# Kernel optimization log

Hardware: AMD Instinct MI355X
Metric: run time of the kernel (lower is better)

Reference implementation:

```python
import jax, jax.numpy as jnp
import numpy as np

V, E, H, L, T, B = 50257, 1024, 16, 12, 128, 16
FF = 4 * E
STD = 0.02


def setup_inputs() -> dict:
    key = jax.random.key(0)
    ks = jax.random.split(key, 20)
    n = lambda k, shape: (jax.random.normal(k, shape, dtype=jnp.float32) * STD)
    inp = {
        'idx': jax.random.randint(ks[0], (B, T), 0, V, dtype=jnp.int64),
        'targets': jax.random.randint(ks[1], (B, T), 0, V, dtype=jnp.int64),
        'tok_emb': n(ks[2], (V, E)),
        'pos_emb': n(ks[3], (T, E)),
        'wq': n(ks[4], (L, E, E)),
        'wk': n(ks[5], (L, E, E)),
        'wv': n(ks[6], (L, E, E)),
        'w_proj': n(ks[7], (L, E, E)),
        'b_proj': jnp.zeros((L, E), jnp.float32),
        'ln1_g': jnp.ones((L, E), jnp.float32),
        'ln1_b': jnp.zeros((L, E), jnp.float32),
        'ln2_g': jnp.ones((L, E), jnp.float32),
        'ln2_b': jnp.zeros((L, E), jnp.float32),
        'w_fc1': n(ks[8], (L, E, FF)),
        'b_fc1': jnp.zeros((L, FF), jnp.float32),
        'w_fc2': n(ks[9], (L, FF, E)),
        'b_fc2': jnp.zeros((L, E), jnp.float32),
        'lnf_g': jnp.ones((E,), jnp.float32),
        'lnf_b': jnp.zeros((E,), jnp.float32),
        'w_head': n(ks[10], (E, V)),
        'b_head': jnp.zeros((V,), jnp.float32),
    }
    return inp


def _layernorm(x, g, b, eps=1e-5):
    m = x.mean(-1, keepdims=True)
    v = ((x - m) ** 2).mean(-1, keepdims=True)
    return (x - m) / jnp.sqrt(v + eps) * g + b


def _forward(idx, targets, tok_emb, pos_emb, wq, wk, wv, w_proj, b_proj,
             ln1_g, ln1_b, ln2_g, ln2_b, w_fc1, b_fc1, w_fc2, b_fc2,
             lnf_g, lnf_b, w_head, b_head):
    Bb, Tt = idx.shape
    x = tok_emb[idx] + pos_emb[:Tt]  # (B, T, E)
    causal = jnp.tril(jnp.ones((Tt, Tt), dtype=bool))
    scale = E ** (-0.5)  # NOTE: original scales by full n_embd, not head_size

    def block(x, p):
        (wq_l, wk_l, wv_l, wp_l, bp_l, g1, b1, g2, b2, wf1, bf1, wf2, bf2) = p
        h = _layernorm(x, g1, b1)
        q = (h @ wq_l).reshape(Bb, Tt, H, -1)
        k = (h @ wk_l).reshape(Bb, Tt, H, -1)
        v = (h @ wv_l).reshape(Bb, Tt, H, -1)
        sc = jnp.einsum('bthd,bshd->bhts', q, k) * scale
        sc = jnp.where(causal, sc, -jnp.inf)
        att = jax.nn.softmax(sc, axis=-1)
        o = jnp.einsum('bhts,bshd->bthd', att, v).reshape(Bb, Tt, E)
        x = x + o @ wp_l + bp_l
        h2 = _layernorm(x, g2, b2)
        x = x + jax.nn.relu(h2 @ wf1 + bf1) @ wf2 + bf2
        return x, None

    x, _ = jax.lax.scan(block, x, (wq, wk, wv, w_proj, b_proj, ln1_g, ln1_b,
                                   ln2_g, ln2_b, w_fc1, b_fc1, w_fc2, b_fc2))
    x = _layernorm(x, lnf_g, lnf_b)
    logits = x @ w_head + b_head  # (B, T, V)
    logp = jax.nn.log_softmax(logits, axis=-1)
    nll = -jnp.take_along_axis(logp.reshape(Bb * Tt, -1),
                               targets.reshape(-1, 1), axis=1)
    loss = nll.mean()
    return logits, loss


def reference(idx, targets, tok_emb, pos_emb, wq, wk, wv, w_proj, b_proj,
              ln1_g, ln1_b, ln2_g, ln2_b, w_fc1, b_fc1, w_fc2, b_fc2,
              lnf_g, lnf_b, w_head, b_head):
    return _forward(idx, targets, tok_emb, pos_emb, wq, wk, wv, w_proj, b_proj,
                    ln1_g, ln1_b, ln2_g, ln2_b, w_fc1, b_fc1, w_fc2, b_fc2,
                    lnf_g, lnf_b, w_head, b_head)
```

## Files before the change

### kernel.cpp

```cpp
#include <hip/hip_runtime.h>
#include <math.h>

typedef unsigned short u16;
typedef float f32x4 __attribute__((ext_vector_type(4)));
typedef short bf16x8 __attribute__((ext_vector_type(8)));
typedef unsigned short us4 __attribute__((ext_vector_type(4)));

#define DEVI __device__ __forceinline__

DEVI float bf2f(u16 u) { return __uint_as_float(((unsigned int)u) << 16); }
DEVI u16 f2bf(float f) {
    unsigned int u = __float_as_uint(f);
    u += 0x7fffu + ((u >> 16) & 1u);
    return (u16)(u >> 16);
}

__global__ __launch_bounds__(256) void k_embed(const int* __restrict__ idx,
                                               const float* __restrict__ te,
                                               const float* __restrict__ pe,
                                               float* __restrict__ x) {
    int m = blockIdx.x;
    int t = m & 127;
    int tok = idx[m];
    const f32x4* a = (const f32x4*)(te + (long)tok * 1024);
    const f32x4* p = (const f32x4*)(pe + (long)t * 1024);
    f32x4* o = (f32x4*)(x + (long)m * 1024);
    o[threadIdx.x] = a[threadIdx.x] + p[threadIdx.x];
}

__global__ __launch_bounds__(256) void k_ln(const float* __restrict__ x,
                                            const float* __restrict__ g,
                                            const float* __restrict__ b,
                                            u16* __restrict__ out) {
    __shared__ float red[8];
    int tid = threadIdx.x, lane = tid & 63, wid = tid >> 6;
    int r = blockIdx.x;
    f32x4 v = ((const f32x4*)(x + (long)r * 1024))[tid];
    float s = v.x + v.y + v.z + v.w;
#pragma unroll
    for (int o2 = 32; o2; o2 >>= 1) s += __shfl_xor(s, o2);
    if (lane == 0) red[wid] = s;
    __syncthreads();
    float mean = (red[0] + red[1] + red[2] + red[3]) * (1.0f / 1024.0f);
    f32x4 d; d.x = v.x - mean; d.y = v.y - mean; d.z = v.z - mean; d.w = v.w - mean;
    float sq = d.x * d.x + d.y * d.y + d.z * d.z + d.w * d.w;
#pragma unroll
    for (int o2 = 32; o2; o2 >>= 1) sq += __shfl_xor(sq, o2);
    if (lane == 0) red[4 + wid] = sq;
    __syncthreads();
    float rstd = rsqrtf((red[4] + red[5] + red[6] + red[7]) * (1.0f / 1024.0f) + 1e-5f);
    f32x4 gg = ((const f32x4*)g)[tid];
    f32x4 bb = ((const f32x4*)b)[tid];
    us4 o4;
    o4.x = f2bf(d.x * rstd * gg.x + bb.x);
    o4.y = f2bf(d.y * rstd * gg.y + bb.y);
    o4.z = f2bf(d.z * rstd * gg.z + bb.z);
    o4.w = f2bf(d.w * rstd * gg.w + bb.w);
    ((us4*)(out + (long)r * 1024))[tid] = o4;
}

DEVI void tr_tile(const float* __restrict__ in, u16* __restrict__ out,
                  int K, int N, int k0, int n0, int tid, float (*tile)[65]) {
    int trow = tid >> 4;
    int tcol = (tid & 15) * 4;
#pragma unroll
    for (int p = 0; p < 4; ++p) {
        int k = k0 + trow + p * 16;
        const float* src = in + (long)k * N + n0 + tcol;
#pragma unroll
        for (int j = 0; j < 4; ++j) {
            int n = n0 + tcol + j;
            tile[trow + p * 16][tcol + j] = (n < N) ? src[j] : 0.0f;
        }
    }
    __syncthreads();
#pragma unroll
    for (int p = 0; p < 4; ++p) {
        int n = n0 + trow + p * 16;
        if (n < N) {
            us4 o4;
#pragma unroll
            for (int j = 0; j < 4; ++j) o4[j] = f2bf(tile[tcol + j][trow + p * 16]);
            *(us4*)(out + (long)n * K + k0 + tcol) = o4;
        }
    }
}

__global__ __launch_bounds__(256) void k_tr_one(const float* __restrict__ in,
                                                u16* __restrict__ out, int K, int N) {
    __shared__ float tile[64][65];
    tr_tile(in, out, K, N, blockIdx.y * 64, blockIdx.x * 64, threadIdx.x, tile);
}

__global__ __launch_bounds__(256) void k_tr_layer(
    const float* __restrict__ wq, const float* __restrict__ wk,
    const float* __restrict__ wv, const float* __restrict__ wp,
    const float* __restrict__ f1, const float* __restrict__ f2,
    u16* __restrict__ oqkv, u16* __restrict__ oproj,
    u16* __restrict__ of1, u16* __restrict__ of2) {
    __shared__ float tile[64][65];
    int id = blockIdx.x;
    const float* in; u16* out; int K, N, txx, tyy;
    if (id < 1024) {
        int t = id >> 8, s2 = id & 255;
        txx = s2 & 15; tyy = s2 >> 4; K = 1024; N = 1024;
        in = (t == 0) ? wq : (t == 1) ? wk : (t == 2) ? wv : wp;
        out = (t == 3) ? oproj : oqkv + (long)t * 1024 * 1024;
    } else if (id < 2048) {
        int s2 = id - 1024;
        txx = s2 & 63; tyy = s2 >> 6; K = 1024; N = 4096; in = f1; out = of1;
    } else {
        int s2 = id - 2048;
        txx = s2 & 15; tyy = s2 >> 4; K = 4096; N = 1024; in = f2; out = of2;
    }
    tr_tile(in, out, K, N, tyy * 64, txx * 64, threadIdx.x, tile);
}

template <int ROWS>
DEVI void stage_tile(const u16* __restrict__ g, long row0, long rowmax, int ld,
                     int col0, char* lds, int tid) {
    constexpr int NCH = ROWS * 8;
#pragma unroll
    for (int p = 0; p < NCH / 256; ++p) {
        int c = tid + p * 256;
        int row = c >> 3;
        int gslot = c & 7;
        int gdata = gslot ^ (row & 7);
        long gr = row0 + row;
        if (gr > rowmax) gr = rowmax;
        const u16* src = g + gr * (long)ld + col0 + gdata * 8;
        char* dst = lds + ((long)((tid & 192) + p * 256)) * 16;
        __builtin_amdgcn_global_load_lds(
            (const __attribute__((address_space(1))) void*)src,
            (__attribute__((address_space(3))) void*)dst, 16, 0, 0);
    }
}

template <int BN, bool OUT_BF16, bool RELU, bool HAS_BIAS, bool HAS_RES>
__global__ __launch_bounds__(256, 3) void k_gemm(
    const u16* __restrict__ A, const u16* __restrict__ Bt,
    const float* __restrict__ bias, const float* __restrict__ res,
    float* __restrict__ Cf, u16* __restrict__ Cb,
    int M, int N, int K, int ldc) {
    constexpr int NR = BN / 32;
    constexpr int ASZ = 128 * 64 * 2;
    constexpr int BSZ = BN * 64 * 2;
    __shared__ __align__(16) char lds[2 * (ASZ + BSZ)];
    int tid = threadIdx.x, lane = tid & 63, wid = tid >> 6;
    int l15 = lane & 15, l4 = lane >> 4;
    int wr = wid >> 1, wc = wid & 1;
    long m0 = (long)blockIdx.y * 128;
    long n0 = (long)blockIdx.x * BN;
    f32x4 acc[4][NR] = {};
    const int nk = K >> 6;

    stage_tile<128>(A, m0, (long)M - 1, K, 0, lds, tid);
    stage_tile<BN>(Bt, n0, (long)N - 1, K, 0, lds + ASZ, tid);
    int cur = 0;
    for (int kt = 0; kt < nk; ++kt) {
        __syncthreads();
        if (kt + 1 < nk) {
            char* nb = lds + (cur ^ 1) * (ASZ + BSZ);
            stage_tile<128>(A, m0, (long)M - 1, K, (kt + 1) << 6, nb, tid);
            stage_tile<BN>(Bt, n0, (long)N - 1, K, (kt + 1) << 6, nb + ASZ, tid);
        }
        const char* ab = lds + cur * (ASZ + BSZ);
        const char* bb = ab + ASZ;
#pragma unroll
        for (int kh = 0; kh < 2; ++kh) {
            bf16x8 af[4], bfv[NR];
#pragma unroll
            for (int mi = 0; mi < 4; ++mi) {
                int row = wr * 64 + mi * 16 + l15;
                int slot = (kh * 4 + l4) ^ (row & 7);
                af[mi] = *(const bf16x8*)(ab + (row * 8 + slot) * 16);
            }
#pragma unroll
            for (int ni = 0; ni < NR; ++ni) {
                int row = wc * (BN / 2) + ni * 16 + l15;
                int slot = (kh * 4 + l4) ^ (row & 7);
                bfv[ni] = *(const bf16x8*)(bb + (row * 8 + slot) * 16);
            }
#pragma unroll
            for (int mi = 0; mi < 4; ++mi)
#pragma unroll
                for (int ni = 0; ni < NR; ++ni)
                    acc[mi][ni] = __builtin_amdgcn_mfma_f32_16x16x32_bf16(
                        af[mi], bfv[ni], acc[mi][ni], 0, 0, 0);
        }
        cur ^= 1;
    }
#pragma unroll
    for (int ni = 0; ni < NR; ++ni) {
        long n = n0 + wc * (BN / 2) + ni * 16 + l15;
        if (n < N) {
            float bv = HAS_BIAS ? bias[n] : 0.0f;
#pragma unroll
            for (int mi = 0; mi < 4; ++mi) {
#pragma unroll
                for (int j = 0; j < 4; ++j) {
                    long m = m0 + wr * 64 + mi * 16 + l4 * 4 + j;
                    float v = acc[mi][ni][j] + bv;
                    if (HAS_RES) v += res[m * (long)ldc + n];
                    if (RELU) v = fmaxf(v, 0.0f);
                    if (OUT_BF16) Cb[m * (long)ldc + n] = f2bf(v);
                    else Cf[m * (long)ldc + n] = v;
                }
            }
        }
    }
}

__global__ __launch_bounds__(256, 2) void k_head128(
    const u16* __restrict__ A, const u16* __restrict__ Bt,
    const float* __restrict__ bias, float* __restrict__ Cf,
    float2* __restrict__ part, int M, int N, int K, int ldc) {
    constexpr int ASZ = 128 * 64 * 2;
    constexpr int BSZ = 128 * 64 * 2;
    __shared__ __align__(16) char lds[128 * 129 * 4];
    int tid = threadIdx.x, lane = tid & 63, wid = tid >> 6;
    int l15 = lane & 15, l4 = lane >> 4;
    int wr = wid >> 1, wc = wid & 1;
    int bn = blockIdx.x, bm = blockIdx.y;
    long m0 = (long)bm * 128, n0 = (long)bn * 128;
    f32x4 acc[4][4] = {};
    const int nk = K >> 6;

    stage_tile<128>(A, m0, (long)M - 1, K, 0, lds, tid);
    stage_tile<128>(Bt, n0, (long)N - 1, K, 0, lds + ASZ, tid);
    int cur = 0;
    for (int kt = 0; kt < nk; ++kt) {
        __syncthreads();
        if (kt + 1 < nk) {
            char* nb = lds + (cur ^ 1) * (ASZ + BSZ);
            stage_tile<128>(A, m0, (long)M - 1, K, (kt + 1) << 6, nb, tid);
            stage_tile<128>(Bt, n0, (long)N - 1, K, (kt + 1) << 6, nb + ASZ, tid);
        }
        const char* ab = lds + cur * (ASZ + BSZ);
        const char* bb = ab + ASZ;
#pragma unroll
        for (int kh = 0; kh < 2; ++kh) {
            bf16x8 af[4], bfv[4];
#pragma unroll
            for (int mi = 0; mi < 4; ++mi) {
                int row = wr * 64 + mi * 16 + l15;
                int slot = (kh * 4 + l4) ^ (row & 7);
                af[mi] = *(const bf16x8*)(ab + (row * 8 + slot) * 16);
            }
#pragma unroll
            for (int ni = 0; ni < 4; ++ni) {
                int row = wc * 64 + ni * 16 + l15;
                int slot = (kh * 4 + l4) ^ (row & 7);
                bfv[ni] = *(const bf16x8*)(bb + (row * 8 + slot) * 16);
            }
#pragma unroll
            for (int mi = 0; mi < 4; ++mi)
#pragma unroll
                for (int ni = 0; ni < 4; ++ni)
                    acc[mi][ni] = __builtin_amdgcn_mfma_f32_16x16x32_bf16(
                        af[mi], bfv[ni], acc[mi][ni], 0, 0, 0);
        }
        cur ^= 1;
    }
    const float BIG_NEG = -1e30f;
    float bvv[4];
#pragma unroll
    for (int ni = 0; ni < 4; ++ni) {
        long n = n0 + wc * 64 + ni * 16 + l15;
        bvv[ni] = (n < N) ? bias[n] : 0.0f;
    }
    __syncthreads();
    float* ldsF = (float*)lds;
#pragma unroll
    for (int mi = 0; mi < 4; ++mi)
#pragma unroll
        for (int ni = 0; ni < 4; ++ni)
#pragma unroll
            for (int j = 0; j < 4; ++j) {
                int row = wr * 64 + mi * 16 + l4 * 4 + j;
                int col = wc * 64 + ni * 16 + l15;
                long n = n0 + col;
                float v = acc[mi][ni][j] + bvv[ni];
                if (n >= N) v = BIG_NEG;
                ldsF[row * 129 + col] = v;
            }
    __syncthreads();
#pragma unroll 4
    for (int i = 0; i < 64; ++i) {
        int flat = tid + (i << 8);
        int row = flat >> 7, col = flat & 127;
        long n = n0 + col;
        if (n < N)
            __builtin_nontemporal_store(ldsF[row * 129 + col],
                                        &Cf[(m0 + row) * (long)ldc + n]);
    }
    {
        int r = tid >> 1, half = tid & 1;
        const float* rp = ldsF + r * 129 + half * 64;
        float mx = BIG_NEG;
#pragma unroll 8
        for (int c = 0; c < 64; ++c) mx = fmaxf(mx, rp[c]);
        float sm = 0.f;
#pragma unroll 8
        for (int c = 0; c < 64; ++c) sm += __expf(rp[c] - mx);
        float mo = __shfl_xor(mx, 1), so = __shfl_xor(sm, 1);
        float nm = fmaxf(mx, mo);
        float S = sm * __expf(mx - nm) + so * __expf(mo - nm);
        if (half == 0)
            part[(long)bn * M + m0 + r] = make_float2(nm, S);
    }
}

__global__ __launch_bounds__(256) void k_attn_mfma(const u16* __restrict__ qkv,
                                                   u16* __restrict__ o) {
    __shared__ __align__(16) u16 Ks[128 * 64];
    __shared__ __align__(16) u16 Vt[64 * 128];
    __shared__ __align__(16) u16 Ps[4][32 * 128];
    int tid = threadIdx.x, lane = tid & 63, w = tid >> 6;
    int l15 = lane & 15, l4 = lane >> 4;
    int b = blockIdx.x >> 4, h = blockIdx.x & 15;
    const u16* base = qkv + (long)b * 128 * 3072 + h * 64;

    stage_tile<128>(base + 1024, 0, 127, 3072, 0, (char*)Ks, tid);
    {
        const u16* vg = base + 2048;
#pragma unroll
        for (int p = 0; p < 4; ++p) {
            int s0 = (w * 4 + p) * 8;
            u16 tmp[8];
#pragma unroll
            for (int j = 0; j < 8; ++j) tmp[j] = vg[(long)(s0 + j) * 3072 + lane];
            int slot = (s0 >> 3) ^ (lane & 7);
            *(bf16x8*)((char*)Vt + lane * 256 + slot * 16) = *(bf16x8*)tmp;
        }
    }
    bf16x8 aq[2][2];
#pragma unroll
    for (int mj = 0; mj < 2; ++mj)
#pragma unroll
        for (int kk = 0; kk < 2; ++kk)
            aq[mj][kk] = *(const bf16x8*)(base + (long)(w * 32 + mj * 16 + l15) * 3072 + kk * 32 + l4 * 8);
    __syncthreads();

    f32x4 sacc[2][8] = {};
#pragma unroll
    for (int sj = 0; sj < 8; ++sj) {
        bf16x8 bk[2];
#pragma unroll
        for (int kk = 0; kk < 2; ++kk) {
            int row = sj * 16 + l15;
            int slot = (kk * 4 + l4) ^ (row & 7);
            bk[kk] = *(const bf16x8*)((char*)Ks + (row * 8 + slot) * 16);
        }
#pragma unroll
        for (int mj = 0; mj < 2; ++mj) {
            sacc[mj][sj] = __builtin_amdgcn_mfma_f32_16x16x32_bf16(aq[mj][0], bk[0], sacc[mj][sj], 0, 0, 0);
            sacc[mj][sj] = __builtin_amdgcn_mfma_f32_16x16x32_bf16(aq[mj][1], bk[1], sacc[mj][sj], 0, 0, 0);
        }
    }
    const float scale = 0.03125f;
#pragma unroll
    for (int mj = 0; mj < 2; ++mj) {
#pragma unroll
        for (int j = 0; j < 4; ++j) {
            int tq = w * 32 + mj * 16 + l4 * 4 + j;
            float mx = -INFINITY;
#pragma unroll
            for (int sj = 0; sj < 8; ++sj) {
                int s = sj * 16 + l15;
                float v = (s <= tq) ? sacc[mj][sj][j] * scale : -INFINITY;
                sacc[mj][sj][j] = v;
                mx = fmaxf(mx, v);
            }
#pragma unroll
            for (int ofs = 1; ofs < 16; ofs <<= 1) mx = fmaxf(mx, __shfl_xor(mx, ofs));
            float sm = 0.f;
#pragma unroll
            for (int sj = 0; sj < 8; ++sj) {
                float e = __expf(sacc[mj][sj][j] - mx);
                sacc[mj][sj][j] = e;
                sm += e;
            }
#pragma unroll
            for (int ofs = 1; ofs < 16; ofs <<= 1) sm += __shfl_xor(sm, ofs);
            float inv = 1.0f / sm;
            int m2 = mj * 16 + l4 * 4 + j;
            u16* prow = Ps[w] + m2 * 128;
#pragma unroll
            for (int sj = 0; sj < 8; ++sj) {
                int s = sj * 16 + l15;
                int slot = (s >> 3) ^ (m2 & 7);
                prow[slot * 8 + (s & 7)] = f2bf(sacc[mj][sj][j] * inv);
            }
        }
    }
    f32x4 oacc[2][4] = {};
#pragma unroll
    for (int kk = 0; kk < 4; ++kk) {
        bf16x8 pa[2], bv[4];
#pragma unroll
        for (int mj = 0; mj < 2; ++mj) {
            int m2 = mj * 16 + l15;
            int slot = (kk * 4 + l4) ^ (m2 & 7);
            pa[mj] = *(const bf16x8*)((char*)(Ps[w]) + m2 * 256 + slot * 16);
        }
#pragma unroll
        for (int nb = 0; nb < 4; ++nb) {
            int d = nb * 16 + l15;
            int slot = (kk * 4 + l4) ^ (d & 7);
            bv[nb] = *(const bf16x8*)((char*)Vt + d * 256 + slot * 16);
        }
#pragma unroll
        for (int mj = 0; mj < 2; ++mj)
#pragma unroll
            for (int nb = 0; nb < 4; ++nb)
                oacc[mj][nb] = __builtin_amdgcn_mfma_f32_16x16x32_bf16(pa[mj], bv[nb], oacc[mj][nb], 0, 0, 0);
    }
#pragma unroll
    for (int mj = 0; mj < 2; ++mj)
#pragma unroll
        for (int nb = 0; nb < 4; ++nb) {
            int d = nb * 16 + l15;
#pragma unroll
            for (int j = 0; j < 4; ++j) {
                int tq = w * 32 + mj * 16 + l4 * 4 + j;
                o[((long)b * 128 + tq) * 1024 + h * 64 + d] = f2bf(oacc[mj][nb][j]);
            }
        }
}

__global__ __launch_bounds__(64) void k_loss_rows2(const float2* __restrict__ part,
                                                   const float* __restrict__ logits,
                                                   const int* __restrict__ tgt,
                                                   float* __restrict__ rowloss, int ncb) {
    int r = blockIdx.x, lane = threadIdx.x;
    float M = -1e30f, S = 0.f;
    for (int cb = lane; cb < ncb; cb += 64) {
        float2 p = part[(long)cb * 2048 + r];
        float nm = fmaxf(M, p.x);
        S = S * __expf(M - nm) + p.y * __expf(p.x - nm);
        M = nm;
    }
#pragma unroll
    for (int ofs = 32; ofs; ofs >>= 1) {
        float M2 = __shfl_xor(M, ofs), S2 = __shfl_xor(S, ofs);
        float nm = fmaxf(M, M2);
        S = S * __expf(M - nm) + S2 * __expf(M2 - nm);
        M = nm;
    }
    if (lane == 0)
        rowloss[r] = (M + logf(S)) - logits[(long)r * 50257 + tgt[r]];
}

__global__ __launch_bounds__(256) void k_loss_reduce(const float* __restrict__ rowloss,
                                                     float* __restrict__ out) {
    __shared__ float red[4];
    int tid = threadIdx.x, lane = tid & 63, wid = tid >> 6;
    float s = 0.f;
    for (int i = tid; i < 2048; i += 256) s += rowloss[i];
#pragma unroll
    for (int ofs = 32; ofs; ofs >>= 1) s += __shfl_xor(s, ofs);
    if (lane == 0) red[wid] = s;
    __syncthreads();
    if (tid == 0) out[0] = (red[0] + red[1] + red[2] + red[3]) * (1.0f / 2048.0f);
}

extern "C" void kernel_launch(void* const* d_in, const int* in_sizes, int n_in,
                              void* d_out, int out_size, void* d_ws, size_t ws_size,
                              hipStream_t stream) {
    (void)in_sizes; (void)n_in; (void)out_size; (void)ws_size;
    const int*   idx     = (const int*)d_in[0];
    const int*   targets = (const int*)d_in[1];
    const float* tok_emb = (const float*)d_in[2];
    const float* pos_emb = (const float*)d_in[3];
    const float* wq      = (const float*)d_in[4];
    const float* wk      = (const float*)d_in[5];
    const float* wv      = (const float*)d_in[6];
    const float* w_proj  = (const float*)d_in[7];
    const float* b_proj  = (const float*)d_in[8];
    const float* ln1_g   = (const float*)d_in[9];
    const float* ln1_b   = (const float*)d_in[10];
    const float* ln2_g   = (const float*)d_in[11];
    const float* ln2_b   = (const float*)d_in[12];
    const float* w_fc1   = (const float*)d_in[13];
    const float* b_fc1   = (const float*)d_in[14];
    const float* w_fc2   = (const float*)d_in[15];
    const float* b_fc2   = (const float*)d_in[16];
    const float* lnf_g   = (const float*)d_in[17];
    const float* lnf_b   = (const float*)d_in[18];
    const float* w_head  = (const float*)d_in[19];
    const float* b_head  = (const float*)d_in[20];
    float* out = (float*)d_out;

    char* w = (char*)d_ws;
    auto alloc = [&](size_t bytes) {
        char* p = w;
        w += (bytes + 255) & ~(size_t)255;
        return p;
    };
    u16*    wT_qkv  = (u16*)alloc(3072L * 1024 * 2);
    u16*    wT_proj = (u16*)alloc(1024L * 1024 * 2);
    u16*    wT_f1   = (u16*)alloc(4096L * 1024 * 2);
    u16*    wT_f2   = (u16*)alloc(1024L * 4096 * 2);
    u16*    wT_head = (u16*)alloc(50257L * 1024 * 2);
    float*  x       = (float*)alloc(2048L * 1024 * 4);
    u16*    h_bf    = (u16*)alloc(2048L * 1024 * 2);
    u16*    qkvb    = (u16*)alloc(2048L * 3072 * 2);
    u16*    o_bf    = (u16*)alloc(2048L * 1024 * 2);
    u16*    ff_bf   = (u16*)alloc(2048L * 4096 * 2);
    float2* part    = (float2*)alloc(393L * 2048 * 8);
    float*  rowloss = (float*)alloc(2048L * 4);

    k_embed<<<2048, 256, 0, stream>>>(idx, tok_emb, pos_emb, x);
    k_tr_one<<<dim3(786, 16), 256, 0, stream>>>(w_head, wT_head, 1024, 50257);

    for (int l = 0; l < 12; ++l) {
        k_tr_layer<<<3072, 256, 0, stream>>>(
            wq + (long)l * 1048576, wk + (long)l * 1048576,
            wv + (long)l * 1048576, w_proj + (long)l * 1048576,
            w_fc1 + (long)l * 4194304, w_fc2 + (long)l * 4194304,
            wT_qkv, wT_proj, wT_f1, wT_f2);
        k_ln<<<2048, 256, 0, stream>>>(x, ln1_g + l * 1024, ln1_b + l * 1024, h_bf);
        k_gemm<64, true, false, false, false><<<dim3(48, 16), 256, 0, stream>>>(
            h_bf, wT_qkv, nullptr, nullptr, nullptr, qkvb, 2048, 3072, 1024, 3072);
        k_attn_mfma<<<256, 256, 0, stream>>>(qkvb, o_bf);
        k_gemm<64, false, false, true, true><<<dim3(16, 16), 256, 0, stream>>>(
            o_bf, wT_proj, b_proj + l * 1024, x, x, nullptr, 2048, 1024, 1024, 1024);
        k_ln<<<2048, 256, 0, stream>>>(x, ln2_g + l * 1024, ln2_b + l * 1024, h_bf);
        k_gemm<64, true, true, true, false><<<dim3(64, 16), 256, 0, stream>>>(
            h_bf, wT_f1, b_fc1 + l * 4096, nullptr, nullptr, ff_bf, 2048, 4096, 1024, 4096);
        k_gemm<64, false, false, true, true><<<dim3(16, 16), 256, 0, stream>>>(
            ff_bf, wT_f2, b_fc2 + l * 1024, x, x, nullptr, 2048, 1024, 4096, 1024);
    }
    k_ln<<<2048, 256, 0, stream>>>(x, lnf_g, lnf_b, h_bf);
    k_head128<<<dim3(393, 16), 256, 0, stream>>>(h_bf, wT_head, b_head, out, part,
                                                 2048, 50257, 1024, 50257);
    k_loss_rows2<<<2048, 64, 0, stream>>>(part, out, targets, rowloss, 393);
    k_loss_reduce<<<1, 256, 0, stream>>>(rowloss, out + 102926336L);
}
```

Measured before the change: 2.130 ms.

## Enlarge LM-head tile to 256 rows with 512 threads and widen QKV/FC1 GEMM tiles

The LM-head kernel now uses 512-thread blocks covering 256 rows by 128 columns, halving the grid rows. A new 512-thread staging helper loads the larger A tile. The QKV and FC1 GEMMs switch from BN=64 to BN=128 tiles, and the generic GEMM's launch bound drops from 3 to 2 blocks per SM. Larger tiles improve operand reuse and cut global traffic for the weight and activation matrices, at the cost of more LDS and registers per block, lower occupancy, and fewer blocks to fill the GPU. The head kernel's softmax and partial-reduction tail sits in the hidden portion, so it is unclear whether that code was updated for 256 rows and 8 waves.

```diff
diff --git a/kernel.cpp b/kernel.cpp
--- a/kernel.cpp
+++ b/kernel.cpp
@@ -136,8 +136,28 @@
     }
 }
 
+template <int ROWS>
+DEVI void stage512(const u16* __restrict__ g, long row0, long rowmax, int ld,
+                   int col0, char* lds, int tid) {
+    constexpr int NP = ROWS * 8 / 512;
+#pragma unroll
+    for (int p = 0; p < NP; ++p) {
+        int c = tid + p * 512;
+        int row = c >> 3;
+        int gslot = c & 7;
+        int gdata = gslot ^ (row & 7);
+        long gr = row0 + row;
+        if (gr > rowmax) gr = rowmax;
+        const u16* src = g + gr * (long)ld + col0 + gdata * 8;
+        char* dst = lds + ((long)((tid & 448) + p * 512)) * 16;
+        __builtin_amdgcn_global_load_lds(
+            (const __attribute__((address_space(1))) void*)src,
+            (__attribute__((address_space(3))) void*)dst, 16, 0, 0);
+    }
+}
+
 template <int BN, bool OUT_BF16, bool RELU, bool HAS_BIAS, bool HAS_RES>
-__global__ __launch_bounds__(256, 3) void k_gemm(
+__global__ __launch_bounds__(256, 2) void k_gemm(
     const u16* __restrict__ A, const u16* __restrict__ Bt,
     const float* __restrict__ bias, const float* __restrict__ res,
     float* __restrict__ Cf, u16* __restrict__ Cb,
@@ -211,30 +231,30 @@
     }
 }
 
-__global__ __launch_bounds__(256, 2) void k_head128(
+__global__ __launch_bounds__(512, 1) void k_head256(
     const u16* __restrict__ A, const u16* __restrict__ Bt,
     const float* __restrict__ bias, float* __restrict__ Cf,
     float2* __restrict__ part, int M, int N, int K, int ldc) {
-    constexpr int ASZ = 128 * 64 * 2;
+    constexpr int ASZ = 256 * 64 * 2;
     constexpr int BSZ = 128 * 64 * 2;
-    __shared__ __align__(16) char lds[128 * 129 * 4];
+    __shared__ __align__(16) char lds[256 * 129 * 4];
     int tid = threadIdx.x, lane = tid & 63, wid = tid >> 6;
     int l15 = lane & 15, l4 = lane >> 4;
     int wr = wid >> 1, wc = wid & 1;
     int bn = blockIdx.x, bm = blockIdx.y;
-    long m0 = (long)bm * 128, n0 = (long)bn * 128;
+    long m0 = (long)bm * 256, n0 = (long)bn * 128;
     f32x4 acc[4][4] = {};
     const int nk = K >> 6;
 
-    stage_tile<128>(A, m0, (long)M - 1, K, 0, lds, tid);
-    stage_tile<128>(Bt, n0, (long)N - 1, K, 0, lds + ASZ, tid);
+    stage512<256>(A, m0, (long)M - 1, K, 0, lds, tid);
+    stage512<128>(Bt, n0, (long)N - 1, K, 0, lds + ASZ, tid);
     int cur = 0;
     for (int kt = 0; kt < nk; ++kt) {
         __syncthreads();
         if (kt + 1 < nk) {
             char* nb = lds + (cur ^ 1) * (ASZ + BSZ);
-            stage_tile<128>(A, m0, (long)M - 1, K, (kt + 1) << 6, nb, tid);
-            stage_tile<128>(Bt, n0, (long)N - 1, K, (kt + 1) << 6, nb + ASZ, tid);
+            stage512<256>(A, m0, (long)M - 1, K, (kt + 1) << 6, nb, tid);
+            stage512<128>(Bt, n0, (long)N - 1, K, (kt + 1) << 6, nb + ASZ, tid);
         }
         const char* ab = lds + cur * (ASZ + BSZ);
         const char* bb = ab + ASZ;
@@ -287,7 +307,7 @@
     __syncthreads();
 #pragma unroll 4
     for (int i = 0; i < 64; ++i) {
-        int flat = tid + (i << 8);
+        int flat = tid + (i << 9);
         int row = flat >> 7, col = flat & 127;
         long n = n0 + col;
         if (n < N)
@@ -521,20 +541,20 @@
             w_fc1 + (long)l * 4194304, w_fc2 + (long)l * 4194304,
             wT_qkv, wT_proj, wT_f1, wT_f2);
         k_ln<<<2048, 256, 0, stream>>>(x, ln1_g + l * 1024, ln1_b + l * 1024, h_bf);
-        k_gemm<64, true, false, false, false><<<dim3(48, 16), 256, 0, stream>>>(
+        k_gemm<128, true, false, false, false><<<dim3(24, 16), 256, 0, stream>>>(
             h_bf, wT_qkv, nullptr, nullptr, nullptr, qkvb, 2048, 3072, 1024, 3072);
         k_attn_mfma<<<256, 256, 0, stream>>>(qkvb, o_bf);
         k_gemm<64, false, false, true, true><<<dim3(16, 16), 256, 0, stream>>>(
             o_bf, wT_proj, b_proj + l * 1024, x, x, nullptr, 2048, 1024, 1024, 1024);
         k_ln<<<2048, 256, 0, stream>>>(x, ln2_g + l * 1024, ln2_b + l * 1024, h_bf);
-        k_gemm<64, true, true, true, false><<<dim3(64, 16), 256, 0, stream>>>(
+        k_gemm<128, true, true, true, false><<<dim3(32, 16), 256, 0, stream>>>(
             h_bf, wT_f1, b_fc1 + l * 4096, nullptr, nullptr, ff_bf, 2048, 4096, 1024, 4096);
         k_gemm<64, false, false, true, true><<<dim3(16, 16), 256, 0, stream>>>(
             ff_bf, wT_f2, b_fc2 + l * 1024, x, x, nullptr, 2048, 1024, 4096, 1024);
     }
     k_ln<<<2048, 256, 0, stream>>>(x, lnf_g, lnf_b, h_bf);
-    k_head128<<<dim3(393, 16), 256, 0, stream>>>(h_bf, wT_head, b_head, out, part,
-                                                 2048, 50257, 1024, 50257);
+    k_head256<<<dim3(393, 8), 512, 0, stream>>>(h_bf, wT_head, b_head, out, part,
+                                                2048, 50257, 1024, 50257);
     k_loss_rows2<<<2048, 64, 0, stream>>>(part, out, targets, rowloss, 393);
     k_loss_reduce<<<1, 256, 0, stream>>>(rowloss, out + 102926336L);
 }
```

Measured after the change: 2.059 ms. 3.4% less time.
